# Kernel tuning notes

Hardware: AMD Instinct MI355X
Metric: run time of the kernel (lower is better)

The kernel has to match this reference:

```python
import jax, jax.numpy as jnp
import numpy as np

N_NODES = 100000
IN_CH = 64
HID = 16
HEADS = 4
OUT_CH = 1
NEG_SLOPE = 0.2
EPS = 1e-16


def gat_conv(x, src, dst, W, att_src, att_dst, bias, heads, out_ch, concat):
    """PyG-style GATConv. src/dst already include self-loops.
    x: [N, F_in]; W: [F_in, heads*out_ch]; att_*: [heads, out_ch]; bias: [heads*out_ch] or [out_ch]."""
    n = x.shape[0]
    h = (x @ W).reshape(n, heads, out_ch)                     # [N,H,C]
    a_src = jnp.einsum('nhc,hc->nh', h, att_src)              # [N,H]
    a_dst = jnp.einsum('nhc,hc->nh', h, att_dst)              # [N,H]
    alpha = jax.nn.leaky_relu(a_src[src] + a_dst[dst], NEG_SLOPE)  # [E,H]
    # segment softmax over incoming edges of each destination node
    m = jax.ops.segment_max(alpha, dst, num_segments=n)       # [N,H]
    e = jnp.exp(alpha - m[dst])
    denom = jax.ops.segment_sum(e, dst, num_segments=n)
    alpha = e / (denom[dst] + EPS)                            # [E,H]
    msg = h[src] * alpha[:, :, None]                          # [E,H,C]
    out = jax.ops.segment_sum(msg, dst, num_segments=n)       # [N,H,C]
    out = out.reshape(n, heads * out_ch) if concat else out.mean(axis=1)
    return out + bias


def setup_inputs() -> dict:
    key = jax.random.key(0)
    ks = jax.random.split(key, 10)
    x = jax.random.normal(ks[0], (N_NODES, IN_CH), dtype=jnp.float32)
    edge_index = jax.random.randint(ks[1], (2, 1600000), 0, N_NODES, dtype=jnp.int64)
    s = 0.1
    W1 = jax.random.normal(ks[2], (IN_CH, HEADS * HID), dtype=jnp.float32) * s
    att_src1 = jax.random.normal(ks[3], (HEADS, HID), dtype=jnp.float32) * s
    att_dst1 = jax.random.normal(ks[4], (HEADS, HID), dtype=jnp.float32) * s
    b1 = jnp.zeros((HEADS * HID,), dtype=jnp.float32)
    W2 = jax.random.normal(ks[5], (HEADS * HID, OUT_CH), dtype=jnp.float32) * s
    att_src2 = jax.random.normal(ks[6], (1, OUT_CH), dtype=jnp.float32) * s
    att_dst2 = jax.random.normal(ks[7], (1, OUT_CH), dtype=jnp.float32) * s
    b2 = jnp.zeros((OUT_CH,), dtype=jnp.float32)
    return {"x": x, "edge_index": edge_index, "W1": W1, "att_src1": att_src1,
            "att_dst1": att_dst1, "b1": b1, "W2": W2, "att_src2": att_src2,
            "att_dst2": att_dst2, "b2": b2}


def reference(x, edge_index, W1, att_src1, att_dst1, b1, W2, att_src2, att_dst2, b2):
    n = x.shape[0]
    loop = jnp.arange(n, dtype=edge_index.dtype)
    src = jnp.concatenate([edge_index[0], loop])  # self-loops (PyG default)
    dst = jnp.concatenate([edge_index[1], loop])
    h = gat_conv(x, src, dst, W1, att_src1, att_dst1, b1, HEADS, HID, concat=True)
    h = jax.nn.elu(h)
    out = gat_conv(h, src, dst, W2, att_src2, att_dst2, b2, 1, OUT_CH, concat=False)
    return out.squeeze()
```

## Files before the change

kernel.cpp:

```cpp
#include <hip/hip_runtime.h>
#include <hip/hip_fp16.h>

#define NN   100000
#define E0   1600000
#define ET   1700000
#define NEG  0.2f
#define EPSV 1e-16f
#define NBK  1563
#define CAP  1536
#define BS   1024
#define NBLK4 ((ET + 4 * BS - 1) / (4 * BS))
#define GEMM_NB 782
#define BC_NB   416
#define E1_NB   6256

typedef _Float16 half8 __attribute__((ext_vector_type(8)));
typedef float f32x16 __attribute__((ext_vector_type(16)));

__global__ __launch_bounds__(256) void k_g1bc(
    const float* __restrict__ x, const int* __restrict__ ei,
    const float* __restrict__ W1, const float* __restrict__ as1,
    const float* __restrict__ ad1,
    __half* __restrict__ h1h, float* __restrict__ asrc1, float* __restrict__ adst1,
    int* __restrict__ bcnt)
{
    int t = threadIdx.x;
    if (blockIdx.x >= GEMM_NB) {
        __shared__ int cnt[NBK];
        for (int i = t; i < NBK; i += 256) cnt[i] = 0;
        __syncthreads();
        int base = (blockIdx.x - GEMM_NB) * (256 * 16);
#pragma unroll
        for (int k = 0; k < 16; ++k) {
            int idx = base + k * 256 + t;
            if (idx < ET) {
                int d = (idx < E0) ? ei[E0 + idx] : (idx - E0);
                atomicAdd(&cnt[d >> 6], 1);
            }
        }
        __syncthreads();
        for (int i = t; i < NBK; i += 256) if (cnt[i]) atomicAdd(&bcnt[i], cnt[i]);
        return;
    }
    __shared__ float Wl[4096];
    __shared__ float Ul[512];
    for (int i = t; i < 4096; i += 256) Wl[i] = W1[i];
    __syncthreads();
    if (t < 64) {
        int k = t;
#pragma unroll
        for (int h = 0; h < 4; ++h) {
            float su = 0.f, du = 0.f;
#pragma unroll
            for (int c = 0; c < 16; ++c) {
                float w = Wl[k * 64 + h * 16 + c];
                su += w * as1[h * 16 + c];
                du += w * ad1[h * 16 + c];
            }
            Ul[k * 8 + h] = su;
            Ul[k * 8 + 4 + h] = du;
        }
    }
    __syncthreads();
    int lane = t & 63, wv = t >> 6;
    int col = lane & 31, q = lane >> 5;
    half8 bf0[4], bf1[4], bf2[4];
#pragma unroll
    for (int kc = 0; kc < 4; ++kc) {
#pragma unroll
        for (int j = 0; j < 8; ++j) {
            int k = kc * 16 + q * 8 + j;
            bf0[kc][j] = (_Float16)Wl[k * 64 + col];
            bf1[kc][j] = (_Float16)Wl[k * 64 + 32 + col];
            bf2[kc][j] = (col < 8) ? (_Float16)Ul[k * 8 + col] : (_Float16)0.f;
        }
    }
    int tile = blockIdx.x * 4 + wv;
    int n0 = tile * 32;
    if (n0 >= NN) return;
    half8 af[4];
    const float* xrow = x + (size_t)(n0 + col) * 64;
#pragma unroll
    for (int kc = 0; kc < 4; ++kc) {
        float4 xa = *(const float4*)(xrow + kc * 16 + q * 8);
        float4 xb = *(const float4*)(xrow + kc * 16 + q * 8 + 4);
        af[kc][0] = (_Float16)xa.x; af[kc][1] = (_Float16)xa.y;
        af[kc][2] = (_Float16)xa.z; af[kc][3] = (_Float16)xa.w;
        af[kc][4] = (_Float16)xb.x; af[kc][5] = (_Float16)xb.y;
        af[kc][6] = (_Float16)xb.z; af[kc][7] = (_Float16)xb.w;
    }
    f32x16 c0 = {}, c1 = {}, c2 = {};
#pragma unroll
    for (int kc = 0; kc < 4; ++kc) {
        c0 = __builtin_amdgcn_mfma_f32_32x32x16_f16(af[kc], bf0[kc], c0, 0, 0, 0);
        c1 = __builtin_amdgcn_mfma_f32_32x32x16_f16(af[kc], bf1[kc], c1, 0, 0, 0);
        c2 = __builtin_amdgcn_mfma_f32_32x32x16_f16(af[kc], bf2[kc], c2, 0, 0, 0);
    }
    int hA = col >> 4, cc = col & 15;
#pragma unroll
    for (int reg = 0; reg < 16; ++reg) {
        int row = (reg & 3) + 8 * (reg >> 2) + 4 * q;
        size_t n = (size_t)(n0 + row);
        h1h[((size_t)hA * NN + n) * 16 + cc]       = __float2half(c0[reg]);
        h1h[((size_t)(hA + 2) * NN + n) * 16 + cc] = __float2half(c1[reg]);
    }
    if (col < 8) {
        float* dst = (col < 4) ? asrc1 : adst1;
        int h = col & 3;
#pragma unroll
        for (int reg = 0; reg < 16; ++reg) {
            int row = (reg & 3) + 8 * (reg >> 2) + 4 * q;
            dst[(size_t)h * NN + (n0 + row)] = c2[reg];
        }
    }
}

__global__ __launch_bounds__(1024) void k_bscan(const int* __restrict__ bcnt,
                                                int* __restrict__ bbase, int* __restrict__ bcursor)
{
    int t = threadIdx.x;
    int i0 = 2 * t, i1 = 2 * t + 1;
    int a = (i0 < NBK) ? bcnt[i0] : 0;
    int b = (i1 < NBK) ? bcnt[i1] : 0;
    int s = a + b;
    int lane = t & 63, wid = t >> 6;
    int sc = s;
#pragma unroll
    for (int off = 1; off < 64; off <<= 1) {
        int u = __shfl_up(sc, off, 64);
        if (lane >= off) sc += u;
    }
    __shared__ int wsum[16];
    if (lane == 63) wsum[wid] = sc;
    __syncthreads();
    int woff = 0;
    for (int k = 0; k < wid; ++k) woff += wsum[k];
    int excl = sc - s + woff;
    if (i0 < NBK) { bbase[i0] = excl;     bcursor[i0] = excl; }
    if (i1 < NBK) { bbase[i1] = excl + a; bcursor[i1] = excl + a; }
}

__global__ __launch_bounds__(BS) void k_bscat(const int* __restrict__ ei,
                                              int* __restrict__ bcursor, int* __restrict__ bin)
{
    __shared__ int cnt[NBK];
    __shared__ int base[NBK];
    int t = threadIdx.x;
    for (int i = t; i < NBK; i += BS) cnt[i] = 0;
    __syncthreads();
    int blk = blockIdx.x * (BS * 4);
    int b[4], r[4], pk[4];
#pragma unroll
    for (int k = 0; k < 4; ++k) {
        int idx = blk + k * BS + t;
        r[k] = -1;
        if (idx < ET) {
            int s, d;
            if (idx < E0) { s = ei[idx]; d = ei[E0 + idx]; } else { s = d = idx - E0; }
            b[k] = d >> 6;
            pk[k] = s | ((d & 63) << 17);
            r[k] = atomicAdd(&cnt[b[k]], 1);
        }
    }
    __syncthreads();
    for (int i = t; i < NBK; i += BS) if (cnt[i]) base[i] = atomicAdd(&bcursor[i], cnt[i]);
    __syncthreads();
#pragma unroll
    for (int k = 0; k < 4; ++k)
        if (r[k] >= 0) bin[base[b[k]] + r[k]] = pk[k];
}

__global__ __launch_bounds__(256) void k_bsort(
    int* __restrict__ bin, const int* __restrict__ bbase, const int* __restrict__ bcnt,
    int* __restrict__ A)
{
    __shared__ int raw[CAP];
    __shared__ int srt[CAP];
    __shared__ int deg[64], cur[64];
    int b = blockIdx.x, t = threadIdx.x;
    int beg = bbase[b], cnt = bcnt[b];
    if (cnt > CAP) cnt = CAP;
    if (t < 64) deg[t] = 0;
    for (int i = t; i < cnt; i += 256) raw[i] = bin[beg + i];
    __syncthreads();
    for (int i = t; i < cnt; i += 256) atomicAdd(&deg[raw[i] >> 17], 1);
    __syncthreads();
    if (t < 64) {
        int v = deg[t];
        int sc = v;
#pragma unroll
        for (int off = 1; off < 64; off <<= 1) {
            int u = __shfl_up(sc, off, 64);
            if (t >= off) sc += u;
        }
        cur[t] = sc - v;
        int n = b * 64 + t;
        if (n < NN) A[n] = beg + sc;
    }
    __syncthreads();
    for (int i = t; i < cnt; i += 256) {
        int e = raw[i];
        int r = atomicAdd(&cur[e >> 17], 1);
        srt[r] = e & 0x1FFFF;
    }
    __syncthreads();
    for (int i = t; i < cnt; i += 256) bin[beg + i] = srt[i];
}

__global__ __launch_bounds__(256) void k_e1agg(
    const int* __restrict__ bin, const int* __restrict__ A,
    const int* __restrict__ bbase, const int* __restrict__ bcnt,
    const float* __restrict__ asrc1, const float* __restrict__ adst1,
    const __half* __restrict__ h1h, const float* __restrict__ b1,
    const float* __restrict__ W2, float* __restrict__ g)
{
    __shared__ int lcsr[CAP];
    int bid = blockIdx.x, t = threadIdx.x;
    int lane8 = bid & 7;
    int h = lane8 >> 1;
    int b = (bid >> 3) * 2 + (lane8 & 1);
    if (b >= NBK) return;
    int beg = bbase[b], cnt = bcnt[b];
    if (cnt > CAP) cnt = CAP;
    for (int i = t; i < cnt; i += 256) lcsr[i] = bin[beg + i];
    __syncthreads();
    int p = t & 3, nl = t >> 2;
    int n = b * 64 + nl;
    if (n >= NN) return;
    int je = A[n] - beg;
    int jb = ((n == 0) ? 0 : A[n - 1]) - beg;
    if (je > cnt) je = cnt;
    if (jb < 0) jb = 0;
    size_t hb = (size_t)h * NN;
    float adv = adst1[hb + n];
    float acc[16];
#pragma unroll
    for (int c = 0; c < 16; ++c) acc[c] = 0.f;
    float den = 0.f;
    for (int j = jb + p; j < je; j += 4) {
        int s = lcsr[j];
        float av = asrc1[hb + s];
        const uint4* hp = (const uint4*)(h1h + (hb + s) * 16);
        uint4 r0 = hp[0], r1 = hp[1];
        float a = av + adv; a = a > 0.f ? a : NEG * a;
        float ev = __expf(a);
        den += ev;
        float2 f0 = __half22float2(*(const __half2*)&r0.x);
        float2 f1 = __half22float2(*(const __half2*)&r0.y);
        float2 f2 = __half22float2(*(const __half2*)&r0.z);
        float2 f3 = __half22float2(*(const __half2*)&r0.w);
        acc[0] += ev * f0.x; acc[1] += ev * f0.y;
        acc[2] += ev * f1.x; acc[3] += ev * f1.y;
        acc[4] += ev * f2.x; acc[5] += ev * f2.y;
        acc[6] += ev * f3.x; acc[7] += ev * f3.y;
        float2 f4 = __half22float2(*(const __half2*)&r1.x);
        float2 f5 = __half22float2(*(const __half2*)&r1.y);
        float2 f6 = __half22float2(*(const __half2*)&r1.z);
        float2 f7 = __half22float2(*(const __half2*)&r1.w);
        acc[8]  += ev * f4.x; acc[9]  += ev * f4.y;
        acc[10] += ev * f5.x; acc[11] += ev * f5.y;
        acc[12] += ev * f6.x; acc[13] += ev * f6.y;
        acc[14] += ev * f7.x; acc[15] += ev * f7.y;
    }
#pragma unroll
    for (int c = 0; c < 16; ++c) {
        acc[c] += __shfl_xor(acc[c], 1);
        acc[c] += __shfl_xor(acc[c], 2);
    }
    den += __shfl_xor(den, 1);
    den += __shfl_xor(den, 2);
    if (p != 0) return;
    float inv = 1.f / (den + EPSV);
    const float4* bp = (const float4*)(b1 + h * 16);
    const float4* wp = (const float4*)(W2 + h * 16);
    float gv = 0.f;
#pragma unroll
    for (int qq = 0; qq < 4; ++qq) {
        float4 bb = bp[qq], w2 = wp[qq];
        float v0 = acc[4*qq+0] * inv + bb.x; v0 = v0 > 0.f ? v0 : __expf(v0) - 1.f;
        float v1 = acc[4*qq+1] * inv + bb.y; v1 = v1 > 0.f ? v1 : __expf(v1) - 1.f;
        float v2 = acc[4*qq+2] * inv + bb.z; v2 = v2 > 0.f ? v2 : __expf(v2) - 1.f;
        float v3 = acc[4*qq+3] * inv + bb.w; v3 = v3 > 0.f ? v3 : __expf(v3) - 1.f;
        gv += v0 * w2.x + v1 * w2.y + v2 * w2.z + v3 * w2.w;
    }
    atomicAdd(&g[n], gv);
}

__global__ __launch_bounds__(256) void k_e2agg(
    const int* __restrict__ bin, const int* __restrict__ A,
    const int* __restrict__ bbase, const int* __restrict__ bcnt,
    const float* __restrict__ g, const float* __restrict__ as2,
    const float* __restrict__ ad2, const float* __restrict__ b2,
    float* __restrict__ out)
{
    __shared__ int lcsr[CAP];
    int b = blockIdx.x, t = threadIdx.x;
    int beg = bbase[b], cnt = bcnt[b];
    if (cnt > CAP) cnt = CAP;
    for (int i = t; i < cnt; i += 256) lcsr[i] = bin[beg + i];
    __syncthreads();
    int p = t & 3, nl = t >> 2;
    int n = b * 64 + nl;
    if (n >= NN) return;
    int je = A[n] - beg;
    int jb = ((n == 0) ? 0 : A[n - 1]) - beg;
    if (je > cnt) je = cnt;
    if (jb < 0) jb = 0;
    float cs = as2[0];
    float gdcd = g[n] * ad2[0];
    float acc = 0.f, den = 0.f;
    for (int j = jb + p; j < je; j += 4) {
        float gz = g[lcsr[j]];
        float a = gz * cs + gdcd;
        a = a > 0.f ? a : NEG * a;
        float ev = __expf(a);
        den += ev;
        acc += ev * gz;
    }
    acc += __shfl_xor(acc, 1); den += __shfl_xor(den, 1);
    acc += __shfl_xor(acc, 2); den += __shfl_xor(den, 2);
    if (p == 0) out[n] = acc / (den + EPSV) + b2[0];
}

extern "C" void kernel_launch(void* const* d_in, const int* in_sizes, int n_in,
                              void* d_out, int out_size, void* d_ws, size_t ws_size,
                              hipStream_t stream)
{
    const float* x   = (const float*)d_in[0];
    const int*   ei  = (const int*)d_in[1];
    const float* W1  = (const float*)d_in[2];
    const float* as1 = (const float*)d_in[3];
    const float* ad1 = (const float*)d_in[4];
    const float* b1  = (const float*)d_in[5];
    const float* W2  = (const float*)d_in[6];
    const float* as2 = (const float*)d_in[7];
    const float* ad2 = (const float*)d_in[8];
    const float* b2  = (const float*)d_in[9];
    float* out = (float*)d_out;

    int*   iw      = (int*)d_ws;
    float* fw      = (float*)d_ws;
    int*   bcnt    = iw;
    int*   bbase   = iw + 1664;
    int*   bcursor = iw + 3328;
    int*   A       = iw + 4992;
    int*   bin     = iw + 105344;
    float* asrcm   = fw + 1805344;
    float* adstm   = fw + 2205344;
    float* g       = fw + 2605344;
    __half* h1hm   = (__half*)(fw + 2705376);

    hipMemsetAsync(bcnt, 0, NBK * sizeof(int), stream);
    hipMemsetAsync(g, 0, NN * sizeof(float), stream);

    k_g1bc  <<<GEMM_NB + BC_NB, 256, 0, stream>>>(x, ei, W1, as1, ad1,
                                                  h1hm, asrcm, adstm, bcnt);
    k_bscan <<<1, 1024, 0, stream>>>(bcnt, bbase, bcursor);
    k_bscat <<<NBLK4, BS, 0, stream>>>(ei, bcursor, bin);
    k_bsort <<<NBK, 256, 0, stream>>>(bin, bbase, bcnt, A);
    k_e1agg <<<E1_NB, 256, 0, stream>>>(bin, A, bbase, bcnt, asrcm, adstm,
                                        h1hm, b1, W2, g);
    k_e2agg <<<NBK, 256, 0, stream>>>(bin, A, bbase, bcnt, g, as2, ad2, b2, out);
}
```

Measured before the change: 222.6 us.

## Precompute per-edge attention weights and softmax denominators in bucket sort kernel

After: 249.6 us. 12.1% more time.

```diff
diff --git a/kernel.cpp b/kernel.cpp
--- a/kernel.cpp
+++ b/kernel.cpp
@@ -21,7 +21,7 @@
     const float* __restrict__ x, const int* __restrict__ ei,
     const float* __restrict__ W1, const float* __restrict__ as1,
     const float* __restrict__ ad1,
-    __half* __restrict__ h1h, float* __restrict__ asrc1, float* __restrict__ adst1,
+    __half* __restrict__ h1h, float* __restrict__ asr, float* __restrict__ adr,
     int* __restrict__ bcnt)
 {
     int t = threadIdx.x;
@@ -105,12 +105,12 @@
         h1h[((size_t)(hA + 2) * NN + n) * 16 + cc] = __float2half(c1[reg]);
     }
     if (col < 8) {
-        float* dst = (col < 4) ? asrc1 : adst1;
+        float* dst = (col < 4) ? asr : adr;
         int h = col & 3;
 #pragma unroll
         for (int reg = 0; reg < 16; ++reg) {
             int row = (reg & 3) + 8 * (reg >> 2) + 4 * q;
-            dst[(size_t)h * NN + (n0 + row)] = c2[reg];
+            dst[(n0 + row) * 4 + h] = c2[reg];
         }
     }
 }
@@ -172,15 +172,26 @@
 
 __global__ __launch_bounds__(256) void k_bsort(
     int* __restrict__ bin, const int* __restrict__ bbase, const int* __restrict__ bcnt,
-    int* __restrict__ A)
+    const float* __restrict__ asr, const float* __restrict__ adr,
+    int* __restrict__ binE01, int* __restrict__ binE23,
+    float* __restrict__ invQ, int* __restrict__ A)
 {
     __shared__ int raw[CAP];
-    __shared__ int srt[CAP];
+    __shared__ int srtS[CAP];
+    __shared__ int srtE01[CAP];
+    __shared__ int srtE23[CAP];
+    __shared__ float adl[256];
+    __shared__ float den[256];
     __shared__ int deg[64], cur[64];
     int b = blockIdx.x, t = threadIdx.x;
     int beg = bbase[b], cnt = bcnt[b];
     if (cnt > CAP) cnt = CAP;
     if (t < 64) deg[t] = 0;
+    den[t] = 0.f;
+    {
+        int gi = b * 256 + t;
+        adl[t] = (gi < NN * 4) ? adr[gi] : 0.f;
+    }
     for (int i = t; i < cnt; i += 256) raw[i] = bin[beg + i];
     __syncthreads();
     for (int i = t; i < cnt; i += 256) atomicAdd(&deg[raw[i] >> 17], 1);
@@ -200,21 +211,49 @@
     __syncthreads();
     for (int i = t; i < cnt; i += 256) {
         int e = raw[i];
-        int r = atomicAdd(&cur[e >> 17], 1);
-        srt[r] = e & 0x1FFFF;
-    }
-    __syncthreads();
-    for (int i = t; i < cnt; i += 256) bin[beg + i] = srt[i];
+        int s = e & 0x1FFFF, dl = e >> 17;
+        int r = atomicAdd(&cur[dl], 1);
+        float4 as4 = *(const float4*)(asr + s * 4);
+        int dl4 = dl * 4;
+        float a0 = as4.x + adl[dl4 + 0]; a0 = a0 > 0.f ? a0 : NEG * a0;
+        float a1 = as4.y + adl[dl4 + 1]; a1 = a1 > 0.f ? a1 : NEG * a1;
+        float a2 = as4.z + adl[dl4 + 2]; a2 = a2 > 0.f ? a2 : NEG * a2;
+        float a3 = as4.w + adl[dl4 + 3]; a3 = a3 > 0.f ? a3 : NEG * a3;
+        __half q0 = __float2half(__expf(a0));
+        __half q1 = __float2half(__expf(a1));
+        __half q2 = __float2half(__expf(a2));
+        __half q3 = __float2half(__expf(a3));
+        atomicAdd(&den[dl4 + 0], __half2float(q0));
+        atomicAdd(&den[dl4 + 1], __half2float(q1));
+        atomicAdd(&den[dl4 + 2], __half2float(q2));
+        atomicAdd(&den[dl4 + 3], __half2float(q3));
+        srtS[r]   = s;
+        srtE01[r] = (int)__half_as_ushort(q0) | ((int)__half_as_ushort(q1) << 16);
+        srtE23[r] = (int)__half_as_ushort(q2) | ((int)__half_as_ushort(q3) << 16);
+    }
+    __syncthreads();
+    for (int i = t; i < cnt; i += 256) {
+        bin[beg + i]    = srtS[i];
+        binE01[beg + i] = srtE01[i];
+        binE23[beg + i] = srtE23[i];
+    }
+    {
+        int nl = t >> 2, h = t & 3;
+        int n = b * 64 + nl;
+        if (n < NN) invQ[(size_t)h * NN + n] = 1.f / (den[nl * 4 + h] + EPSV);
+    }
 }
 
 __global__ __launch_bounds__(256) void k_e1agg(
-    const int* __restrict__ bin, const int* __restrict__ A,
+    const int* __restrict__ binS, const int* __restrict__ binE01,
+    const int* __restrict__ binE23, const int* __restrict__ A,
     const int* __restrict__ bbase, const int* __restrict__ bcnt,
-    const float* __restrict__ asrc1, const float* __restrict__ adst1,
-    const __half* __restrict__ h1h, const float* __restrict__ b1,
-    const float* __restrict__ W2, float* __restrict__ g)
-{
-    __shared__ int lcsr[CAP];
+    const __half* __restrict__ h1h, const float* __restrict__ invQ,
+    const float* __restrict__ b1, const float* __restrict__ W2,
+    float* __restrict__ g)
+{
+    __shared__ int lS[CAP];
+    __shared__ int lE[CAP];
     int bid = blockIdx.x, t = threadIdx.x;
     int lane8 = bid & 7;
     int h = lane8 >> 1;
@@ -222,72 +261,57 @@
     if (b >= NBK) return;
     int beg = bbase[b], cnt = bcnt[b];
     if (cnt > CAP) cnt = CAP;
-    for (int i = t; i < cnt; i += 256) lcsr[i] = bin[beg + i];
-    __syncthreads();
-    int p = t & 3, nl = t >> 2;
+    const int* binE = (h < 2) ? binE01 : binE23;
+    for (int i = t; i < cnt; i += 256) { lS[i] = binS[beg + i]; lE[i] = binE[beg + i]; }
+    __syncthreads();
+    int q = t & 3, nl = t >> 2;
     int n = b * 64 + nl;
     if (n >= NN) return;
-    int je = A[n] - beg;
-    int jb = ((n == 0) ? 0 : A[n - 1]) - beg;
-    if (je > cnt) je = cnt;
-    if (jb < 0) jb = 0;
+    int je = A[n] - beg;               if (je > cnt) je = cnt;
+    int jb = ((n == 0) ? 0 : A[n - 1]) - beg; if (jb < 0) jb = 0;
     size_t hb = (size_t)h * NN;
-    float adv = adst1[hb + n];
-    float acc[16];
-#pragma unroll
-    for (int c = 0; c < 16; ++c) acc[c] = 0.f;
-    float den = 0.f;
-    for (int j = jb + p; j < je; j += 4) {
-        int s = lcsr[j];
-        float av = asrc1[hb + s];
-        const uint4* hp = (const uint4*)(h1h + (hb + s) * 16);
-        uint4 r0 = hp[0], r1 = hp[1];
-        float a = av + adv; a = a > 0.f ? a : NEG * a;
-        float ev = __expf(a);
-        den += ev;
-        float2 f0 = __half22float2(*(const __half2*)&r0.x);
-        float2 f1 = __half22float2(*(const __half2*)&r0.y);
-        float2 f2 = __half22float2(*(const __half2*)&r0.z);
-        float2 f3 = __half22float2(*(const __half2*)&r0.w);
-        acc[0] += ev * f0.x; acc[1] += ev * f0.y;
-        acc[2] += ev * f1.x; acc[3] += ev * f1.y;
-        acc[4] += ev * f2.x; acc[5] += ev * f2.y;
-        acc[6] += ev * f3.x; acc[7] += ev * f3.y;
-        float2 f4 = __half22float2(*(const __half2*)&r1.x);
-        float2 f5 = __half22float2(*(const __half2*)&r1.y);
-        float2 f6 = __half22float2(*(const __half2*)&r1.z);
-        float2 f7 = __half22float2(*(const __half2*)&r1.w);
-        acc[8]  += ev * f4.x; acc[9]  += ev * f4.y;
-        acc[10] += ev * f5.x; acc[11] += ev * f5.y;
-        acc[12] += ev * f6.x; acc[13] += ev * f6.y;
-        acc[14] += ev * f7.x; acc[15] += ev * f7.y;
-    }
-#pragma unroll
-    for (int c = 0; c < 16; ++c) {
-        acc[c] += __shfl_xor(acc[c], 1);
-        acc[c] += __shfl_xor(acc[c], 2);
-    }
-    den += __shfl_xor(den, 1);
-    den += __shfl_xor(den, 2);
-    if (p != 0) return;
-    float inv = 1.f / (den + EPSV);
-    const float4* bp = (const float4*)(b1 + h * 16);
-    const float4* wp = (const float4*)(W2 + h * 16);
+    int p = q & 1, eo = q >> 1;
+    int hsel = h & 1;
+    float acc[8];
+#pragma unroll
+    for (int c = 0; c < 8; ++c) acc[c] = 0.f;
+    for (int base = jb; base < je; base += 2) {
+        int e = base + eo;
+        if (e < je) {
+            int s = lS[e];
+            int ew = lE[e];
+            unsigned short us = hsel ? (unsigned short)(ew >> 16)
+                                     : (unsigned short)(ew & 0xFFFF);
+            float evf = __half2float(__ushort_as_half(us));
+            uint4 r0 = *(const uint4*)(h1h + (hb + s) * 16 + p * 8);
+            float2 f0 = __half22float2(*(const __half2*)&r0.x);
+            float2 f1 = __half22float2(*(const __half2*)&r0.y);
+            float2 f2 = __half22float2(*(const __half2*)&r0.z);
+            float2 f3 = __half22float2(*(const __half2*)&r0.w);
+            acc[0] += evf * f0.x; acc[1] += evf * f0.y;
+            acc[2] += evf * f1.x; acc[3] += evf * f1.y;
+            acc[4] += evf * f2.x; acc[5] += evf * f2.y;
+            acc[6] += evf * f3.x; acc[7] += evf * f3.y;
+        }
+    }
+#pragma unroll
+    for (int c = 0; c < 8; ++c) acc[c] += __shfl_xor(acc[c], 2);
+    float inv = invQ[hb + n];
+    const float* bp = b1 + h * 16 + p * 8;
+    const float* wp = W2 + h * 16 + p * 8;
     float gv = 0.f;
 #pragma unroll
-    for (int qq = 0; qq < 4; ++qq) {
-        float4 bb = bp[qq], w2 = wp[qq];
-        float v0 = acc[4*qq+0] * inv + bb.x; v0 = v0 > 0.f ? v0 : __expf(v0) - 1.f;
-        float v1 = acc[4*qq+1] * inv + bb.y; v1 = v1 > 0.f ? v1 : __expf(v1) - 1.f;
-        float v2 = acc[4*qq+2] * inv + bb.z; v2 = v2 > 0.f ? v2 : __expf(v2) - 1.f;
-        float v3 = acc[4*qq+3] * inv + bb.w; v3 = v3 > 0.f ? v3 : __expf(v3) - 1.f;
-        gv += v0 * w2.x + v1 * w2.y + v2 * w2.z + v3 * w2.w;
-    }
-    atomicAdd(&g[n], gv);
+    for (int c = 0; c < 8; ++c) {
+        float v = acc[c] * inv + bp[c];
+        v = v > 0.f ? v : __expf(v) - 1.f;
+        gv += v * wp[c];
+    }
+    gv += __shfl_xor(gv, 1);
+    if (q == 0) atomicAdd(&g[n], gv);
 }
 
 __global__ __launch_bounds__(256) void k_e2agg(
-    const int* __restrict__ bin, const int* __restrict__ A,
+    const int* __restrict__ binS, const int* __restrict__ A,
     const int* __restrict__ bbase, const int* __restrict__ bcnt,
     const float* __restrict__ g, const float* __restrict__ as2,
     const float* __restrict__ ad2, const float* __restrict__ b2,
@@ -297,15 +321,13 @@
     int b = blockIdx.x, t = threadIdx.x;
     int beg = bbase[b], cnt = bcnt[b];
     if (cnt > CAP) cnt = CAP;
-    for (int i = t; i < cnt; i += 256) lcsr[i] = bin[beg + i];
+    for (int i = t; i < cnt; i += 256) lcsr[i] = binS[beg + i];
     __syncthreads();
     int p = t & 3, nl = t >> 2;
     int n = b * 64 + nl;
     if (n >= NN) return;
-    int je = A[n] - beg;
-    int jb = ((n == 0) ? 0 : A[n - 1]) - beg;
-    if (je > cnt) je = cnt;
-    if (jb < 0) jb = 0;
+    int je = A[n] - beg;               if (je > cnt) je = cnt;
+    int jb = ((n == 0) ? 0 : A[n - 1]) - beg; if (jb < 0) jb = 0;
     float cs = as2[0];
     float gdcd = g[n] * ad2[0];
     float acc = 0.f, den = 0.f;
@@ -345,20 +367,24 @@
     int*   bcursor = iw + 3328;
     int*   A       = iw + 4992;
     int*   bin     = iw + 105344;
-    float* asrcm   = fw + 1805344;
-    float* adstm   = fw + 2205344;
-    float* g       = fw + 2605344;
-    __half* h1hm   = (__half*)(fw + 2705376);
+    int*   binE01  = iw + 1805344;
+    int*   binE23  = iw + 3505344;
+    float* asr     = fw + 5205344;
+    float* adr     = fw + 5605344;
+    float* invQ    = fw + 6005344;
+    float* g       = fw + 6405344;
+    __half* h1hQ   = (__half*)(fw + 6505376);
 
     hipMemsetAsync(bcnt, 0, NBK * sizeof(int), stream);
     hipMemsetAsync(g, 0, NN * sizeof(float), stream);
 
     k_g1bc  <<<GEMM_NB + BC_NB, 256, 0, stream>>>(x, ei, W1, as1, ad1,
-                                                  h1hm, asrcm, adstm, bcnt);
+                                                  h1hQ, asr, adr, bcnt);
     k_bscan <<<1, 1024, 0, stream>>>(bcnt, bbase, bcursor);
     k_bscat <<<NBLK4, BS, 0, stream>>>(ei, bcursor, bin);
-    k_bsort <<<NBK, 256, 0, stream>>>(bin, bbase, bcnt, A);
-    k_e1agg <<<E1_NB, 256, 0, stream>>>(bin, A, bbase, bcnt, asrcm, adstm,
-                                        h1hm, b1, W2, g);
+    k_bsort <<<NBK, 256, 0, stream>>>(bin, bbase, bcnt, asr, adr,
+                                      binE01, binE23, invQ, A);
+    k_e1agg <<<E1_NB, 256, 0, stream>>>(bin, binE01, binE23, A, bbase, bcnt,
+                                        h1hQ, invQ, b1, W2, g);
     k_e2agg <<<NBK, 256, 0, stream>>>(bin, A, bbase, bcnt, g, as2, ad2, b2, out);
 }
```
